# Performance work log

Hardware: AMD Instinct MI355X
Metric: run time of the kernel (lower is better)

Reference implementation:

```python
import jax, jax.numpy as jnp
import numpy as np

B, S, D, H, WIDTH = 4, 1024, 1024, 16, 32
DEPTH = D // H


def _build_graph(size, width, seed=0):
    # Faithful vectorized port of sparse_attention_graph
    rng = np.random.default_rng(seed)
    normal_pulls = rng.normal(0.0, 1.0 / size, (size, width // 2)) * (size * 1.3)
    nums = normal_pulls.astype(np.int32)
    positions = nums % size
    rows = np.repeat(np.arange(size), width // 2)
    cols = (positions.reshape(-1) + rows) % size
    adjm = np.zeros((size, size), dtype=np.float32)
    adjm[rows, cols] = 1.0
    adjm = np.clip(adjm + adjm.T, a_min=None, a_max=1.0)
    return jnp.asarray(adjm)


def setup_inputs() -> dict:
    key = jax.random.key(0)
    ks = jax.random.split(key, 10)
    inp = {
        'v': jax.random.normal(ks[0], (B, S, D), jnp.float32),
        'q': jax.random.normal(ks[1], (B, S, D), jnp.float32),
        'k': jax.random.normal(ks[2], (B, S, D), jnp.float32),
        'mask': jax.random.randint(ks[3], (B, 1, S, S), 0, 2, jnp.int32),
        'G': _build_graph(D, WIDTH),
        'wq': jax.random.normal(ks[4], (D, D), jnp.float32) * 0.02,
        'bq': jnp.zeros((D,), jnp.float32),
        'wk': jax.random.normal(ks[5], (D, D), jnp.float32) * 0.02,
        'bk': jnp.zeros((D,), jnp.float32),
        'wv': jax.random.normal(ks[6], (D, D), jnp.float32) * 0.02,
        'bv': jnp.zeros((D,), jnp.float32),
        'wo': jax.random.normal(ks[7], (D, D), jnp.float32) * 0.02,
        'bo': jnp.zeros((D,), jnp.float32),
    }
    return inp


def _split_heads(x):
    # [B,S,D] -> [B,H,S,depth]
    b = x.shape[0]
    return x.reshape(b, -1, H, DEPTH).transpose(0, 2, 1, 3)


def reference(v, q, k, mask, G, wq, bq, wk, bk, wv, bv, wo, bo):
    qh = _split_heads(q @ wq + bq)   # [B,H,S,dp]
    kh = _split_heads(k @ wk + bk)
    vh = _split_heads(v @ wv + bv)
    # kg = K^T @ G : [B,H,dp,S]
    kg = jnp.einsum('bhsd,st->bhdt', kh, G)
    # qkg = Q @ kg : [B,H,S,S]
    s = jnp.einsum('bhsd,bhdt->bhst', qh, kg) / jnp.sqrt(jnp.float32(DEPTH))
    s = s - 100000.0 * mask.astype(s.dtype)
    attn_weights = jax.nn.softmax(s, axis=-1)
    attn = jnp.einsum('bhst,bhtd->bhsd', attn_weights, vh)
    attn = attn.transpose(0, 2, 1, 3).reshape(q.shape[0], -1, D)
    output = attn @ wo + bo
    return (output, attn_weights)
```

## Files before the change

### kernel.cpp

```cpp
#include <hip/hip_runtime.h>
#include <cstdint>
#include <cstddef>

#define AS1 __attribute__((address_space(1)))
#define AS3 __attribute__((address_space(3)))

typedef __bf16 bf16x8 __attribute__((ext_vector_type(8)));
typedef __bf16 bf16x4 __attribute__((ext_vector_type(4)));
typedef float  f32x4  __attribute__((ext_vector_type(4)));

namespace {

constexpr int NB = 4;
constexpr int S  = 1024;
constexpr int D  = 1024;
constexpr int NH = 16;
constexpr int DP = 64;

__global__ void __launch_bounds__(256) split_k(const float* __restrict__ src,
                                               __bf16* __restrict__ hi,
                                               __bf16* __restrict__ lo,
                                               size_t n4) {
  size_t i = (size_t)blockIdx.x * blockDim.x + threadIdx.x;
  const size_t stride = (size_t)gridDim.x * blockDim.x;
  for (; i < n4; i += stride) {
    const float4 v = ((const float4*)src)[i];
    bf16x4 h;
    h[0] = (__bf16)v.x; h[1] = (__bf16)v.y; h[2] = (__bf16)v.z; h[3] = (__bf16)v.w;
    ((bf16x4*)hi)[i] = h;
    if (lo != nullptr) {
      bf16x4 l;
      l[0] = (__bf16)(v.x - (float)h[0]);
      l[1] = (__bf16)(v.y - (float)h[1]);
      l[2] = (__bf16)(v.z - (float)h[2]);
      l[3] = (__bf16)(v.w - (float)h[3]);
      ((bf16x4*)lo)[i] = l;
    }
  }
}

__global__ void __launch_bounds__(256) split3_k(const float* __restrict__ s0,
                                                const float* __restrict__ s1,
                                                const float* __restrict__ s2,
                                                __bf16* __restrict__ hi0, size_t n4) {
  const float* srcs[3] = {s0, s1, s2};
  const float* src = srcs[blockIdx.z];
  __bf16* hi = hi0 + (size_t)blockIdx.z * 8388608;
  __bf16* lo = hi + 4194304;
  size_t i = (size_t)blockIdx.x * blockDim.x + threadIdx.x;
  const size_t stride = (size_t)gridDim.x * blockDim.x;
  for (; i < n4; i += stride) {
    const float4 v = ((const float4*)src)[i];
    bf16x4 h, l;
    h[0] = (__bf16)v.x; h[1] = (__bf16)v.y; h[2] = (__bf16)v.z; h[3] = (__bf16)v.w;
    l[0] = (__bf16)(v.x - (float)h[0]);
    l[1] = (__bf16)(v.y - (float)h[1]);
    l[2] = (__bf16)(v.z - (float)h[2]);
    l[3] = (__bf16)(v.w - (float)h[3]);
    ((bf16x4*)hi)[i] = h;
    ((bf16x4*)lo)[i] = l;
  }
}

__global__ void __launch_bounds__(256) tsplit4_k(const float* __restrict__ s0,
                                                 const float* __restrict__ s1,
                                                 const float* __restrict__ s2,
                                                 const float* __restrict__ s3,
                                                 __bf16* __restrict__ hi0) {
  __shared__ float tile[32][33];
  const float* srcs[4] = {s0, s1, s2, s3};
  const float* sp = srcs[blockIdx.z];
  __bf16* hp = hi0 + (size_t)blockIdx.z * 2097152;
  __bf16* lp = hp + 1048576;
  const int r0 = blockIdx.y * 32, c0 = blockIdx.x * 32;
  const int tx = threadIdx.x, ty = threadIdx.y;
  #pragma unroll
  for (int rr = ty; rr < 32; rr += 8)
    tile[rr][tx] = sp[(size_t)(r0 + rr) * D + c0 + tx];
  __syncthreads();
  #pragma unroll
  for (int cc = ty; cc < 32; cc += 8) {
    const float v = tile[tx][cc];
    const __bf16 h = (__bf16)v;
    const size_t o = (size_t)(c0 + cc) * D + r0 + tx;
    hp[o] = h;
    lp[o] = (__bf16)(v - (float)h);
  }
}

__global__ void __launch_bounds__(256) softmax_k(float* __restrict__ aw,
                                                 __bf16* __restrict__ awh) {
  const size_t row = blockIdx.x;
  float* p = aw + row * 1024;
  const int tid = threadIdx.x;
  float4 v = ((const float4*)p)[tid];
  float m = fmaxf(fmaxf(v.x, v.y), fmaxf(v.z, v.w));
  #pragma unroll
  for (int off = 32; off > 0; off >>= 1) m = fmaxf(m, __shfl_xor(m, off));
  __shared__ float red[8];
  const int wv = tid >> 6, ln = tid & 63;
  if (ln == 0) red[wv] = m;
  __syncthreads();
  m = fmaxf(fmaxf(red[0], red[1]), fmaxf(red[2], red[3]));
  const float e0 = __expf(v.x - m), e1 = __expf(v.y - m);
  const float e2 = __expf(v.z - m), e3 = __expf(v.w - m);
  float s = (e0 + e1) + (e2 + e3);
  #pragma unroll
  for (int off = 32; off > 0; off >>= 1) s += __shfl_xor(s, off);
  if (ln == 0) red[4 + wv] = s;
  __syncthreads();
  s = (red[4] + red[5]) + (red[6] + red[7]);
  const float inv = 1.0f / s;
  float4 o; o.x = e0 * inv; o.y = e1 * inv; o.z = e2 * inv; o.w = e3 * inv;
  ((float4*)p)[tid] = o;
  bf16x4 hb;
  hb[0] = (__bf16)o.x; hb[1] = (__bf16)o.y; hb[2] = (__bf16)o.z; hb[3] = (__bf16)o.w;
  ((bf16x4*)(awh + row * 1024))[tid] = hb;
}

struct GemmArgs {
  const __bf16 *Ah, *Al, *Bh, *Bl;
  float* C; __bf16* Chi; __bf16* Clo;
  const float* bias; const int* mask;
  int N, K, ZH;
  long long lda, ldb, ldc;
  long long sAb, sAh, sBb, sBh, sCb, sCh, sMb;
};

template<int BM, int BN, int WM, int WN, bool A_LO, bool B_LO, int EPI>
__global__ void __launch_bounds__(WM * WN * 64) gemm_k(GemmArgs g) {
  constexpr int NW = WM * WN, NT = NW * 64, BK = 32;
  constexpr int WMsz = BM / WM, WNsz = BN / WN;
  constexpr int FM = WMsz / 16, FN = WNsz / 16;
  static_assert((BM * BK / 8) % NT == 0 && (BN * BK / 8) % NT == 0, "stage divisibility");

  __shared__ __attribute__((aligned(16))) __bf16 Ash[BM * BK];
  __shared__ __attribute__((aligned(16))) __bf16 Asl[A_LO ? BM * BK : 8];
  __shared__ __attribute__((aligned(16))) __bf16 Bsh[BN * BK];
  __shared__ __attribute__((aligned(16))) __bf16 Bsl[B_LO ? BN * BK : 8];

  const int tid = threadIdx.x, wave = tid >> 6, lane = tid & 63;
  const int z = blockIdx.z;
  const int zb = z / g.ZH, zh = z - zb * g.ZH;

  const __bf16* Ah = g.Ah + (size_t)zb * g.sAb + (size_t)zh * g.sAh;
  const __bf16* Al = A_LO ? g.Al + (size_t)zb * g.sAb + (size_t)zh * g.sAh : nullptr;
  const __bf16* Bh = g.Bh + (size_t)zb * g.sBb + (size_t)zh * g.sBh;
  const __bf16* Bl = B_LO ? g.Bl + (size_t)zb * g.sBb + (size_t)zh * g.sBh : nullptr;
  float* C = (EPI == 0 || EPI == 2) ? g.C + (size_t)zb * g.sCb + (size_t)zh * g.sCh : nullptr;
  __bf16* Chi = (EPI == 3) ? g.Chi + (size_t)zb * g.sCb + (size_t)zh * g.sCh
                           : g.Chi;
  __bf16* Clo = (EPI == 3) ? g.Clo + (size_t)zb * g.sCb + (size_t)zh * g.sCh
                           : g.Clo;
  const int* mk = (EPI == 2) ? g.mask + (size_t)zb * g.sMb : nullptr;

  const int m0 = blockIdx.y * BM, n0 = blockIdx.x * BN;
  const int wm = wave / WN, wn = wave % WN;
  const int lc = lane & 15;
  const int lkb = (lane >> 4) * 8;
  const int lr4 = (lane >> 4) * 4;

  f32x4 acc[FM][FN] = {};

  for (int k0 = 0; k0 < g.K; k0 += BK) {
    {
      constexpr int ITA = (BM * BK / 8) / NT;
      #pragma unroll
      for (int i = 0; i < ITA; ++i) {
        const int cb = (i * NW + wave) * 64;
        const int ch = cb + lane;
        const int row = ch >> 2, c8 = ch & 3;
        const size_t go = (size_t)(m0 + row) * g.lda + k0 + c8 * 8;
        __builtin_amdgcn_global_load_lds((AS1 void*)(Ah + go),
                                         (AS3 void*)(&Ash[cb * 8]), 16, 0, 0);
        if constexpr (A_LO)
          __builtin_amdgcn_global_load_lds((AS1 void*)(Al + go),
                                           (AS3 void*)(&Asl[cb * 8]), 16, 0, 0);
      }
    }
    {
      constexpr int ITB = (BN * BK / 8) / NT;
      #pragma unroll
      for (int i = 0; i < ITB; ++i) {
        const int cb = (i * NW + wave) * 64;
        const int ch = cb + lane;
        const int row = ch >> 2, c8 = ch & 3;
        const size_t go = (size_t)(n0 + row) * g.ldb + k0 + c8 * 8;
        __builtin_amdgcn_global_load_lds((AS1 void*)(Bh + go),
                                         (AS3 void*)(&Bsh[cb * 8]), 16, 0, 0);
        if constexpr (B_LO)
          __builtin_amdgcn_global_load_lds((AS1 void*)(Bl + go),
                                           (AS3 void*)(&Bsl[cb * 8]), 16, 0, 0);
      }
    }
    __syncthreads();

    bf16x8 ah[FM], al[FM], bh[FN], bl[FN];
    #pragma unroll
    for (int i = 0; i < FM; ++i) {
      const int r = wm * WMsz + i * 16 + lc;
      ah[i] = *(const bf16x8*)&Ash[r * BK + lkb];
      if constexpr (A_LO) al[i] = *(const bf16x8*)&Asl[r * BK + lkb];
    }
    #pragma unroll
    for (int j = 0; j < FN; ++j) {
      const int r = wn * WNsz + j * 16 + lc;
      bh[j] = *(const bf16x8*)&Bsh[r * BK + lkb];
      if constexpr (B_LO) bl[j] = *(const bf16x8*)&Bsl[r * BK + lkb];
    }
    #pragma unroll
    for (int i = 0; i < FM; ++i)
      #pragma unroll
      for (int j = 0; j < FN; ++j) {
        acc[i][j] = __builtin_amdgcn_mfma_f32_16x16x32_bf16(ah[i], bh[j], acc[i][j], 0, 0, 0);
        if constexpr (B_LO)
          acc[i][j] = __builtin_amdgcn_mfma_f32_16x16x32_bf16(ah[i], bl[j], acc[i][j], 0, 0, 0);
        if constexpr (A_LO)
          acc[i][j] = __builtin_amdgcn_mfma_f32_16x16x32_bf16(al[i], bh[j], acc[i][j], 0, 0, 0);
      }
    __syncthreads();
  }

  #pragma unroll
  for (int i = 0; i < FM; ++i)
    #pragma unroll
    for (int j = 0; j < FN; ++j) {
      const int row = m0 + wm * WMsz + i * 16 + lr4;
      const int col = n0 + wn * WNsz + j * 16 + lc;
      float v[4];
      #pragma unroll
      for (int r = 0; r < 4; ++r) v[r] = acc[i][j][r];
      if constexpr (EPI != 2) {
        if (g.bias != nullptr) {
          const float b = g.bias[col];
          #pragma unroll
          for (int r = 0; r < 4; ++r) v[r] += b;
        }
      }
      if constexpr (EPI == 0) {
        #pragma unroll
        for (int r = 0; r < 4; ++r)
          C[(size_t)(row + r) * g.ldc + col] = v[r];
      }
      if constexpr (EPI == 2) {
        #pragma unroll
        for (int r = 0; r < 4; ++r)
          C[(size_t)(row + r) * g.ldc + col] =
              v[r] * 0.125f - 100000.0f * (float)mk[(size_t)(row + r) * g.N + col];
      }
      if constexpr (EPI == 3) {
        #pragma unroll
        for (int r = 0; r < 4; ++r) {
          const __bf16 h = (__bf16)v[r];
          const size_t o = (size_t)(row + r) * g.ldc + col;
          Chi[o] = h;
          Clo[o] = (__bf16)(v[r] - (float)h);
        }
      }
      if constexpr (EPI == 4) {
        bf16x4 h4, l4;
        #pragma unroll
        for (int r = 0; r < 4; ++r) {
          h4[r] = (__bf16)v[r];
          l4[r] = (__bf16)(v[r] - (float)h4[r]);
        }
        const size_t b = (size_t)(row >> 10), rr = row & 1023;
        const size_t o = b * g.sCb + (size_t)col * g.ldc + rr;
        *(bf16x4*)&Chi[o] = h4;
        *(bf16x4*)&Clo[o] = l4;
      }
    }
}

}

extern "C" void kernel_launch(void* const* d_in, const int* in_sizes, int n_in,
                              void* d_out, int out_size, void* d_ws, size_t ws_size,
                              hipStream_t stream) {
  (void)in_sizes; (void)n_in; (void)out_size; (void)ws_size;

  const float* v_in = (const float*)d_in[0];
  const float* q_in = (const float*)d_in[1];
  const float* k_in = (const float*)d_in[2];
  const int*   mask = (const int*)d_in[3];
  const float* Gm   = (const float*)d_in[4];
  const float* wq = (const float*)d_in[5];  const float* bq = (const float*)d_in[6];
  const float* wk = (const float*)d_in[7];  const float* bk = (const float*)d_in[8];
  const float* wv = (const float*)d_in[9];  const float* bv = (const float*)d_in[10];
  const float* wo = (const float*)d_in[11]; const float* bo = (const float*)d_in[12];

  float* out = (float*)d_out;
  float* aw  = out + (size_t)NB * S * D;

  char* ws = (char*)d_ws;
  auto BF = [&](size_t mb) { return (__bf16*)(ws + (mb << 20)); };

  const size_t BSD = (size_t)NB * S * D;

  split3_k<<<dim3(1024, 1, 3), 256, 0, stream>>>(q_in, k_in, v_in, BF(0), BSD / 4);
  split_k<<<1024, 256, 0, stream>>>(Gm, BF(112), nullptr, (size_t)S * S / 4);
  tsplit4_k<<<dim3(32, 32, 4), dim3(32, 8), 0, stream>>>(wq, wk, wv, wo, BF(48));

  GemmArgs pa{};
  pa.N = D; pa.K = D; pa.ZH = 1;
  pa.lda = D; pa.ldb = D; pa.ldc = D;
  pa.Ah = BF(0);  pa.Al = BF(8);  pa.Bh = BF(48); pa.Bl = BF(50);
  pa.Chi = BF(64); pa.Clo = BF(72); pa.bias = bq;
  gemm_k<128, 128, 2, 2, true, true, 3><<<dim3(8, 32, 1), 256, 0, stream>>>(pa);
  pa.Ah = BF(16); pa.Al = BF(24); pa.Bh = BF(52); pa.Bl = BF(54);
  pa.Chi = BF(80); pa.Clo = BF(88); pa.bias = bk;
  pa.ldc = S; pa.sCb = (long long)D * S;
  gemm_k<128, 128, 2, 2, true, true, 4><<<dim3(8, 32, 1), 256, 0, stream>>>(pa);
  pa.Ah = BF(32); pa.Al = BF(40); pa.Bh = BF(56); pa.Bl = BF(58);
  pa.Chi = BF(96); pa.Clo = BF(104); pa.bias = bv;
  gemm_k<128, 128, 2, 2, true, true, 4><<<dim3(8, 32, 1), 256, 0, stream>>>(pa);

  GemmArgs ka{};
  ka.N = D; ka.K = S; ka.ZH = 1;
  ka.lda = S; ka.ldb = S; ka.ldc = D;
  ka.sBb = (long long)D * S; ka.sCb = (long long)S * D;
  ka.Ah = BF(112); ka.Bh = BF(80); ka.Bl = BF(88);
  ka.Chi = BF(114); ka.Clo = BF(122); ka.bias = nullptr;
  gemm_k<128, 128, 2, 2, false, true, 3><<<dim3(8, 8, NB), 256, 0, stream>>>(ka);

  GemmArgs sa{};
  sa.N = S; sa.K = DP; sa.ZH = NH;
  sa.lda = D; sa.ldb = D; sa.ldc = S;
  sa.sAb = (long long)S * D; sa.sAh = DP;
  sa.sBb = (long long)S * D; sa.sBh = DP;
  sa.sCb = (long long)NH * S * S; sa.sCh = (long long)S * S;
  sa.sMb = (long long)S * S;
  sa.Ah = BF(64); sa.Al = BF(72); sa.Bh = BF(114); sa.Bl = BF(122);
  sa.C = aw; sa.mask = mask;
  gemm_k<128, 128, 2, 2, true, true, 2><<<dim3(8, 8, NB * NH), 256, 0, stream>>>(sa);

  softmax_k<<<NB * NH * S, 256, 0, stream>>>(aw, BF(146));

  GemmArgs va{};
  va.N = DP; va.K = S; va.ZH = NH;
  va.lda = S; va.ldb = S; va.ldc = D;
  va.sAb = (long long)NH * S * S; va.sAh = (long long)S * S;
  va.sBb = (long long)D * S;      va.sBh = (long long)DP * S;
  va.sCb = (long long)S * D;      va.sCh = DP;
  va.Ah = BF(146); va.Bh = BF(96); va.Bl = BF(104);
  va.Chi = BF(130); va.Clo = BF(138); va.bias = nullptr;
  gemm_k<128, 64, 2, 2, false, true, 3><<<dim3(1, 8, NB * NH), 256, 0, stream>>>(va);

  GemmArgs fa{};
  fa.N = D; fa.K = D; fa.ZH = 1;
  fa.lda = D; fa.ldb = D; fa.ldc = D;
  fa.Ah = BF(130); fa.Al = BF(138); fa.Bh = BF(60); fa.Bl = BF(62);
  fa.C = out; fa.bias = bo;
  gemm_k<128, 128, 2, 2, true, true, 0><<<dim3(8, 32, 1), 256, 0, stream>>>(fa);
}
```

Measured before the change: 865.7 us.

## Double-buffer GEMM LDS stages, merge K/V projections, shrink tiles for occupancy

The GEMM main loop now uses two LDS buffers and issues the global-to-LDS loads for the next K-slice before the MFMAs on the current one, so load latency overlaps with compute. The K and V projection GEMMs are merged into a single launch over z=2, with a second bias pointer and per-z output offsets. Several GEMMs use 64-row tiles to double the block count. The cost is twice the LDS footprint per block, which may lower occupancy, and a merge that relies on the workspace strides lining up exactly.

```diff
diff --git a/kernel.cpp b/kernel.cpp
--- a/kernel.cpp
+++ b/kernel.cpp
@@ -121,7 +121,7 @@
 struct GemmArgs {
   const __bf16 *Ah, *Al, *Bh, *Bl;
   float* C; __bf16* Chi; __bf16* Clo;
-  const float* bias; const int* mask;
+  const float* bias; const float* bias2; const int* mask;
   int N, K, ZH;
   long long lda, ldb, ldc;
   long long sAb, sAh, sBb, sBh, sCb, sCh, sMb;
@@ -132,12 +132,13 @@
   constexpr int NW = WM * WN, NT = NW * 64, BK = 32;
   constexpr int WMsz = BM / WM, WNsz = BN / WN;
   constexpr int FM = WMsz / 16, FN = WNsz / 16;
-  static_assert((BM * BK / 8) % NT == 0 && (BN * BK / 8) % NT == 0, "stage divisibility");
-
-  __shared__ __attribute__((aligned(16))) __bf16 Ash[BM * BK];
-  __shared__ __attribute__((aligned(16))) __bf16 Asl[A_LO ? BM * BK : 8];
-  __shared__ __attribute__((aligned(16))) __bf16 Bsh[BN * BK];
-  __shared__ __attribute__((aligned(16))) __bf16 Bsl[B_LO ? BN * BK : 8];
+  constexpr int ASZ = BM * BK, BSZ = BN * BK;
+  static_assert((ASZ / 8) % NT == 0 && (BSZ / 8) % NT == 0, "stage divisibility");
+
+  __shared__ __attribute__((aligned(16))) __bf16 Ash[2][ASZ];
+  __shared__ __attribute__((aligned(16))) __bf16 Asl[2][A_LO ? ASZ : 8];
+  __shared__ __attribute__((aligned(16))) __bf16 Bsh[2][BSZ];
+  __shared__ __attribute__((aligned(16))) __bf16 Bsl[2][B_LO ? BSZ : 8];
 
   const int tid = threadIdx.x, wave = tid >> 6, lane = tid & 63;
   const int z = blockIdx.z;
@@ -148,11 +149,17 @@
   const __bf16* Bh = g.Bh + (size_t)zb * g.sBb + (size_t)zh * g.sBh;
   const __bf16* Bl = B_LO ? g.Bl + (size_t)zb * g.sBb + (size_t)zh * g.sBh : nullptr;
   float* C = (EPI == 0 || EPI == 2) ? g.C + (size_t)zb * g.sCb + (size_t)zh * g.sCh : nullptr;
-  __bf16* Chi = (EPI == 3) ? g.Chi + (size_t)zb * g.sCb + (size_t)zh * g.sCh
-                           : g.Chi;
-  __bf16* Clo = (EPI == 3) ? g.Clo + (size_t)zb * g.sCb + (size_t)zh * g.sCh
-                           : g.Clo;
+  __bf16* Chi = g.Chi; __bf16* Clo = g.Clo;
+  if constexpr (EPI == 3) {
+    Chi += (size_t)zb * g.sCb + (size_t)zh * g.sCh;
+    Clo += (size_t)zb * g.sCb + (size_t)zh * g.sCh;
+  }
+  if constexpr (EPI == 4) {
+    Chi += (size_t)zb * g.sCh;
+    Clo += (size_t)zb * g.sCh;
+  }
   const int* mk = (EPI == 2) ? g.mask + (size_t)zb * g.sMb : nullptr;
+  const float* bias = (g.bias2 != nullptr && zb == 1) ? g.bias2 : g.bias;
 
   const int m0 = blockIdx.y * BM, n0 = blockIdx.x * BN;
   const int wm = wave / WN, wn = wave % WN;
@@ -160,54 +167,56 @@
   const int lkb = (lane >> 4) * 8;
   const int lr4 = (lane >> 4) * 4;
 
+  auto stage = [&](int buf, int k0) {
+    constexpr int ITA = (ASZ / 8) / NT;
+    #pragma unroll
+    for (int i = 0; i < ITA; ++i) {
+      const int cb = (i * NW + wave) * 64;
+      const int ch = cb + lane;
+      const int row = ch >> 2, c8 = ch & 3;
+      const size_t go = (size_t)(m0 + row) * g.lda + k0 + c8 * 8;
+      __builtin_amdgcn_global_load_lds((AS1 void*)(Ah + go),
+                                       (AS3 void*)(&Ash[buf][cb * 8]), 16, 0, 0);
+      if constexpr (A_LO)
+        __builtin_amdgcn_global_load_lds((AS1 void*)(Al + go),
+                                         (AS3 void*)(&Asl[buf][cb * 8]), 16, 0, 0);
+    }
+    constexpr int ITB = (BSZ / 8) / NT;
+    #pragma unroll
+    for (int i = 0; i < ITB; ++i) {
+      const int cb = (i * NW + wave) * 64;
+      const int ch = cb + lane;
+      const int row = ch >> 2, c8 = ch & 3;
+      const size_t go = (size_t)(n0 + row) * g.ldb + k0 + c8 * 8;
+      __builtin_amdgcn_global_load_lds((AS1 void*)(Bh + go),
+                                       (AS3 void*)(&Bsh[buf][cb * 8]), 16, 0, 0);
+      if constexpr (B_LO)
+        __builtin_amdgcn_global_load_lds((AS1 void*)(Bl + go),
+                                         (AS3 void*)(&Bsl[buf][cb * 8]), 16, 0, 0);
+    }
+  };
+
   f32x4 acc[FM][FN] = {};
 
-  for (int k0 = 0; k0 < g.K; k0 += BK) {
-    {
-      constexpr int ITA = (BM * BK / 8) / NT;
-      #pragma unroll
-      for (int i = 0; i < ITA; ++i) {
-        const int cb = (i * NW + wave) * 64;
-        const int ch = cb + lane;
-        const int row = ch >> 2, c8 = ch & 3;
-        const size_t go = (size_t)(m0 + row) * g.lda + k0 + c8 * 8;
-        __builtin_amdgcn_global_load_lds((AS1 void*)(Ah + go),
-                                         (AS3 void*)(&Ash[cb * 8]), 16, 0, 0);
-        if constexpr (A_LO)
-          __builtin_amdgcn_global_load_lds((AS1 void*)(Al + go),
-                                           (AS3 void*)(&Asl[cb * 8]), 16, 0, 0);
-      }
-    }
-    {
-      constexpr int ITB = (BN * BK / 8) / NT;
-      #pragma unroll
-      for (int i = 0; i < ITB; ++i) {
-        const int cb = (i * NW + wave) * 64;
-        const int ch = cb + lane;
-        const int row = ch >> 2, c8 = ch & 3;
-        const size_t go = (size_t)(n0 + row) * g.ldb + k0 + c8 * 8;
-        __builtin_amdgcn_global_load_lds((AS1 void*)(Bh + go),
-                                         (AS3 void*)(&Bsh[cb * 8]), 16, 0, 0);
-        if constexpr (B_LO)
-          __builtin_amdgcn_global_load_lds((AS1 void*)(Bl + go),
-                                           (AS3 void*)(&Bsl[cb * 8]), 16, 0, 0);
-      }
-    }
-    __syncthreads();
-
+  stage(0, 0);
+  __syncthreads();
+  int cur = 0;
+  const int nk = g.K / BK;
+  for (int t = 0; t < nk; ++t) {
     bf16x8 ah[FM], al[FM], bh[FN], bl[FN];
     #pragma unroll
     for (int i = 0; i < FM; ++i) {
       const int r = wm * WMsz + i * 16 + lc;
-      ah[i] = *(const bf16x8*)&Ash[r * BK + lkb];
-      if constexpr (A_LO) al[i] = *(const bf16x8*)&Asl[r * BK + lkb];
+      ah[i] = *(const bf16x8*)&Ash[cur][r * BK + lkb];
+      if constexpr (A_LO) al[i] = *(const bf16x8*)&Asl[cur][r * BK + lkb];
     }
     #pragma unroll
     for (int j = 0; j < FN; ++j) {
       const int r = wn * WNsz + j * 16 + lc;
-      bh[j] = *(const bf16x8*)&Bsh[r * BK + lkb];
-      if constexpr (B_LO) bl[j] = *(const bf16x8*)&Bsl[r * BK + lkb];
-    }
+      bh[j] = *(const bf16x8*)&Bsh[cur][r * BK + lkb];
+      if constexpr (B_LO) bl[j] = *(const bf16x8*)&Bsl[cur][r * BK + lkb];
+    }
+    if (t + 1 < nk) stage(cur ^ 1, (t + 1) * BK);
     #pragma unroll
     for (int i = 0; i < FM; ++i)
       #pragma unroll
@@ -219,6 +228,7 @@
           acc[i][j] = __builtin_amdgcn_mfma_f32_16x16x32_bf16(al[i], bh[j], acc[i][j], 0, 0, 0);
       }
     __syncthreads();
+    cur ^= 1;
   }
 
   #pragma unroll
@@ -231,8 +241,8 @@
       #pragma unroll
       for (int r = 0; r < 4; ++r) v[r] = acc[i][j][r];
       if constexpr (EPI != 2) {
-        if (g.bias != nullptr) {
-          const float b = g.bias[col];
+        if (bias != nullptr) {
+          const float b = bias[col];
           #pragma unroll
           for (int r = 0; r < 4; ++r) v[r] += b;
         }
@@ -306,22 +316,27 @@
   pa.lda = D; pa.ldb = D; pa.ldc = D;
   pa.Ah = BF(0);  pa.Al = BF(8);  pa.Bh = BF(48); pa.Bl = BF(50);
   pa.Chi = BF(64); pa.Clo = BF(72); pa.bias = bq;
-  gemm_k<128, 128, 2, 2, true, true, 3><<<dim3(8, 32, 1), 256, 0, stream>>>(pa);
-  pa.Ah = BF(16); pa.Al = BF(24); pa.Bh = BF(52); pa.Bl = BF(54);
-  pa.Chi = BF(80); pa.Clo = BF(88); pa.bias = bk;
-  pa.ldc = S; pa.sCb = (long long)D * S;
-  gemm_k<128, 128, 2, 2, true, true, 4><<<dim3(8, 32, 1), 256, 0, stream>>>(pa);
-  pa.Ah = BF(32); pa.Al = BF(40); pa.Bh = BF(56); pa.Bl = BF(58);
-  pa.Chi = BF(96); pa.Clo = BF(104); pa.bias = bv;
-  gemm_k<128, 128, 2, 2, true, true, 4><<<dim3(8, 32, 1), 256, 0, stream>>>(pa);
+  gemm_k<64, 128, 2, 2, true, true, 3><<<dim3(8, 64, 1), 256, 0, stream>>>(pa);
+
+  GemmArgs kv{};
+  kv.N = D; kv.K = D; kv.ZH = 1;
+  kv.lda = D; kv.ldb = D; kv.ldc = S;
+  kv.Ah = BF(16); kv.Al = BF(24); kv.sAb = 8388608;
+  kv.Bh = BF(52); kv.Bl = BF(54); kv.sBb = 2097152;
+  kv.Chi = BF(80); kv.Clo = BF(88);
+  kv.sCh = 8388608;
+  kv.sCb = (long long)D * S;
+  kv.bias = bk; kv.bias2 = bv;
+  gemm_k<128, 128, 2, 2, true, true, 4><<<dim3(8, 32, 2), 256, 0, stream>>>(kv);
 
   GemmArgs ka{};
   ka.N = D; ka.K = S; ka.ZH = 1;
   ka.lda = S; ka.ldb = S; ka.ldc = D;
+  ka.sAb = 0;
   ka.sBb = (long long)D * S; ka.sCb = (long long)S * D;
   ka.Ah = BF(112); ka.Bh = BF(80); ka.Bl = BF(88);
-  ka.Chi = BF(114); ka.Clo = BF(122); ka.bias = nullptr;
-  gemm_k<128, 128, 2, 2, false, true, 3><<<dim3(8, 8, NB), 256, 0, stream>>>(ka);
+  ka.Chi = BF(114); ka.Clo = BF(122);
+  gemm_k<64, 128, 2, 2, false, true, 3><<<dim3(8, 16, NB), 256, 0, stream>>>(ka);
 
   GemmArgs sa{};
   sa.N = S; sa.K = DP; sa.ZH = NH;
@@ -343,7 +358,7 @@
   va.sBb = (long long)D * S;      va.sBh = (long long)DP * S;
   va.sCb = (long long)S * D;      va.sCh = DP;
   va.Ah = BF(146); va.Bh = BF(96); va.Bl = BF(104);
-  va.Chi = BF(130); va.Clo = BF(138); va.bias = nullptr;
+  va.Chi = BF(130); va.Clo = BF(138);
   gemm_k<128, 64, 2, 2, false, true, 3><<<dim3(1, 8, NB * NH), 256, 0, stream>>>(va);
 
   GemmArgs fa{};
@@ -351,5 +366,5 @@
   fa.lda = D; fa.ldb = D; fa.ldc = D;
   fa.Ah = BF(130); fa.Al = BF(138); fa.Bh = BF(60); fa.Bl = BF(62);
   fa.C = out; fa.bias = bo;
-  gemm_k<128, 128, 2, 2, true, true, 0><<<dim3(8, 32, 1), 256, 0, stream>>>(fa);
-}
+  gemm_k<64, 128, 2, 2, true, true, 0><<<dim3(8, 64, 1), 256, 0, stream>>>(fa);
+}
```

Result: faster. 772.2 us (-10.8%).
